# Optimization experiments

Hardware: AMD Instinct MI355X
Metric: run time of the kernel (lower is better)

## Reference

```python
import jax, jax.numpy as jnp
import numpy as np

K = 1024       # npoint (downsampled points)
NN = 16        # nneighbor (kNN group size)
EPS = 1e-5     # BatchNorm eps


def setup_inputs() -> dict:
    key = jax.random.key(0)
    ks = jax.random.split(key, 6)
    B, N, D = 8, 4096, 64          # channels[0] = D + 3 = 67
    C1, C2 = 128, 128              # mlp = channels[1:]
    xyz = jax.random.normal(ks[0], (B, N, 3), jnp.float32)
    points = jax.random.normal(ks[1], (B, N, D), jnp.float32)
    W1 = jax.random.normal(ks[2], (C1, D + 3), jnp.float32) / np.float32(np.sqrt(D + 3))
    b1 = jnp.zeros((C1,), jnp.float32)
    g1 = jnp.ones((C1,), jnp.float32)
    be1 = jnp.zeros((C1,), jnp.float32)
    W2 = jax.random.normal(ks[3], (C2, C1), jnp.float32) / np.float32(np.sqrt(C1))
    b2 = jnp.zeros((C2,), jnp.float32)
    g2 = jnp.ones((C2,), jnp.float32)
    be2 = jnp.zeros((C2,), jnp.float32)
    return {"xyz": xyz, "points": points, "W1": W1, "b1": b1, "g1": g1, "be1": be1,
            "W2": W2, "b2": b2, "g2": g2, "be2": be2}


def _fps(xyz, npoint):
    # Farthest point sampling: sequential selection via lax.scan.
    B, N, _ = xyz.shape
    def step(carry, _):
        dist, far = carry
        centroid = jnp.take_along_axis(xyz, far[:, None, None], axis=1)  # [B,1,3]
        d = jnp.sum((xyz - centroid) ** 2, axis=-1)                      # [B,N]
        dist = jnp.minimum(dist, d)
        return (dist, jnp.argmax(dist, axis=-1).astype(jnp.int32)), far
    init = (jnp.full((B, N), 1e10, xyz.dtype), jnp.zeros((B,), jnp.int32))
    _, idx = jax.lax.scan(step, init, None, length=npoint)
    return idx.T  # [B, npoint]


def _bn_relu(x, g, b):
    # training-mode BatchNorm2d over (batch, npoint, nsample), per channel (last dim)
    mean = jnp.mean(x, axis=(0, 1, 2), keepdims=True)
    var = jnp.var(x, axis=(0, 1, 2), keepdims=True)
    return jax.nn.relu((x - mean) * jax.lax.rsqrt(var + EPS) * g + b)


def reference(xyz, points, W1, b1, g1, be1, W2, b2, g2, be2):
    B, N, _ = xyz.shape
    fps_idx = _fps(xyz, K)                                  # [B,K]
    gather = jax.vmap(lambda a, i: a[i])
    new_xyz = gather(xyz, fps_idx)                          # [B,K,3]
    # kNN: squared distances from sampled centers to all points
    sq = (jnp.sum(new_xyz ** 2, -1)[:, :, None]
          + jnp.sum(xyz ** 2, -1)[:, None, :]
          - 2.0 * jnp.einsum('bkc,bnc->bkn', new_xyz, xyz))  # [B,K,N]
    _, knn_idx = jax.lax.top_k(-sq, NN)                     # [B,K,NN]
    grouped_xyz = gather(xyz, knn_idx)                      # [B,K,NN,3]
    grouped_xyz = grouped_xyz - new_xyz[:, :, None, :]
    grouped_pts = gather(points, knn_idx)                   # [B,K,NN,D]
    h = jnp.concatenate([grouped_xyz, grouped_pts], axis=-1)  # [B,K,NN,D+3]
    h = _bn_relu(jnp.einsum('bknc,oc->bkno', h, W1) + b1, g1, be1)
    h = _bn_relu(jnp.einsum('bknc,oc->bkno', h, W2) + b2, g2, be2)
    new_points = jnp.max(h, axis=2)                         # [B,K,C2]
    return new_xyz, new_points
```

## Files before the change

kernel.cpp:

```cpp
#include <hip/hip_runtime.h>

#define B_ 8
#define N_ 4096
#define K_ 1024
#define NN_ 16
#define C1_ 128
#define C2_ 128
#define CIN_ 67
#define NROWS (B_*K_*NN_)
#define NBLK  (NROWS/64)
#define NBLK2 (NROWS/32)
#define BN_N 131072.0f

typedef unsigned short u16;

__device__ u16   g_knn[NROWS];
__device__ float g_statsA[8*256];
__device__ float g_statsB[8*256];
__device__ float g_m2[B_*K_*C2_];
__device__ float g_W1T[68*128];
__device__ float g_W2T[128*128];
__device__ __align__(16) float g_h1[(size_t)NROWS*128];

template<int CTRL>
static __device__ __forceinline__ void dpp_maxv_step(float& v) {
    int vi = __float_as_int(v);
    int ov = __builtin_amdgcn_update_dpp(vi, vi, CTRL, 0xf, 0xf, false);
    v = fmaxf(v, __int_as_float(ov));
}
static __device__ __forceinline__ void wave_reduce_maxval(float& v) {
    dpp_maxv_step<0x111>(v);
    dpp_maxv_step<0x112>(v);
    dpp_maxv_step<0x114>(v);
    dpp_maxv_step<0x118>(v);
    dpp_maxv_step<0x142>(v);
    dpp_maxv_step<0x143>(v);
}
template<int CTRL>
static __device__ __forceinline__ void dpp_min_step(float& v, int& ib) {
    int vi = __float_as_int(v);
    int ov = __builtin_amdgcn_update_dpp(vi, vi, CTRL, 0xf, 0xf, false);
    int oi = __builtin_amdgcn_update_dpp(ib, ib, CTRL, 0xf, 0xf, false);
    float of = __int_as_float(ov);
    if (of < v || (of == v && oi < ib)) { v = of; ib = oi; }
}
static __device__ __forceinline__ void wave_reduce_min(float& v, int& ib) {
    dpp_min_step<0x111>(v, ib);
    dpp_min_step<0x112>(v, ib);
    dpp_min_step<0x114>(v, ib);
    dpp_min_step<0x118>(v, ib);
    dpp_min_step<0x142>(v, ib);
    dpp_min_step<0x143>(v, ib);
}

__global__ void transpose_w_kernel(const float* __restrict__ W1,
                                   const float* __restrict__ W2) {
    int t = blockIdx.x * 256 + threadIdx.x;
    if (t < 8*256) { g_statsA[t] = 0.f; g_statsB[t] = 0.f; }
    if (t < 68*128) {
        int q = t >> 7, o = t & 127;
        g_W1T[t] = (q < CIN_) ? W1[o*CIN_ + q] : 0.f;
    }
    if (t < 128*128) {
        int q = t >> 7, o = t & 127;
        g_W2T[t] = W2[o*C1_ + q];
    }
}

__global__ __launch_bounds__(256) void fps_kernel(const float* __restrict__ xyz,
                                                  float* __restrict__ out_xyz) {
    __shared__ float sx[N_*3];
    __shared__ float sout[K_*3];
    __shared__ float wv[2][4];
    __shared__ int   wi[2][4];
    const int b = blockIdx.x, t = threadIdx.x;
    const int l = t & 63, w = t >> 6;
    const float* xb = xyz + b * (N_ * 3);
    for (int e = t; e < N_*3; e += 256) sx[e] = xb[e];
    __syncthreads();
    float x0[16], y0[16], z0[16], dist[16];
    #pragma unroll
    for (int j = 0; j < 16; ++j) {
        int p = t * 16 + j;
        x0[j] = sx[p*3+0]; y0[j] = sx[p*3+1]; z0[j] = sx[p*3+2];
        dist[j] = 1e10f;
    }
    int far = 0;
    for (int s = 0; s < K_; ++s) {
        const float cx = sx[far*3+0], cy = sx[far*3+1], cz = sx[far*3+2];
        if (t == 0) {
            sout[s*3+0] = cx; sout[s*3+1] = cy; sout[s*3+2] = cz;
        }
        float v = -1.f; int ib = 0;
        {
            #pragma clang fp contract(fast)
            #pragma unroll
            for (int j = 0; j < 16; ++j) {
                float dx = x0[j]-cx, dy = y0[j]-cy, dz = z0[j]-cz;
                float dd = dx*dx + dy*dy + dz*dz;
                dd = fminf(dist[j], dd);
                dist[j] = dd;
                if (dd > v) { v = dd; ib = t*16 + j; }
            }
        }
        float vr = v;
        wave_reduce_maxval(vr);
        const float m = __int_as_float(__builtin_amdgcn_readlane(__float_as_int(vr), 63));
        unsigned long long mk = __ballot(v == m);
        const int ln  = __ffsll((unsigned long long)mk) - 1;
        const int wib = __builtin_amdgcn_readlane(ib, ln);
        const int pb = s & 1;
        if (l == 0) { wv[pb][w] = m; wi[pb][w] = wib; }
        __syncthreads();
        float bv = wv[pb][0]; int bi = wi[pb][0];
        #pragma unroll
        for (int ww = 1; ww < 4; ++ww) {
            float ov = wv[pb][ww];
            if (ov > bv) { bv = ov; bi = wi[pb][ww]; }
        }
        far = bi & 4095;
    }
    __syncthreads();
    for (int e = t; e < K_*3; e += 256) out_xyz[b*K_*3 + e] = sout[e];
}

__global__ __launch_bounds__(256) void knn_kernel(const float* __restrict__ xyz,
                                                  const float* __restrict__ newxyz) {
    __shared__ float px[N_], py[N_], pz[N_];
    const int b = blockIdx.y, t = threadIdx.x;
    const int l = t & 63, w = t >> 6;
    const int k = blockIdx.x * 4 + w;
    const int m = b*K_ + k;
    const float* xb = xyz + b * (N_ * 3);
    for (int p = t; p < N_; p += 256) {
        px[p] = xb[p*3+0]; py[p] = xb[p*3+1]; pz[p] = xb[p*3+2];
    }
    __syncthreads();
    const float cx = newxyz[m*3+0];
    const float cy = newxyz[m*3+1];
    const float cz = newxyz[m*3+2];
    float d[64];
    {
        #pragma clang fp contract(off)
        float sn = cx*cx; sn = sn + cy*cy; sn = sn + cz*cz;
        #pragma unroll
        for (int j = 0; j < 64; ++j) {
            int p = j*64 + l;
            float X = px[p], Y = py[p], Z = pz[p];
            float sp = X*X; sp = sp + Y*Y; sp = sp + Z*Z;
            float dt = cx*X; dt = dt + cy*Y; dt = dt + cz*Z;
            float t1 = sn + sp;
            d[j] = t1 - 2.0f*dt;
        }
    }
    float prevd = -1e38f; int previ = -1;
    for (int r = 0; r < NN_; ++r) {
        float bv = 1e38f; int bi = 0x7fffffff;
        #pragma unroll
        for (int j = 0; j < 64; ++j) {
            int p = j*64 + l;
            bool gt = (d[j] > prevd) || (d[j] == prevd && p > previ);
            bool lt = (d[j] < bv)   || (d[j] == bv   && p < bi);
            if (gt && lt) { bv = d[j]; bi = p; }
        }
        wave_reduce_min(bv, bi);
        previ = __builtin_amdgcn_readlane(bi, 63);
        prevd = __int_as_float(__builtin_amdgcn_readlane(__float_as_int(bv), 63));
        if (l == 0) g_knn[m*NN_ + r] = (u16)(previ & 4095);
    }
}

__global__ __launch_bounds__(256) void stats1_kernel(
        const float* __restrict__ xyz, const float* __restrict__ points,
        const float* __restrict__ newxyz, const float* __restrict__ b1) {
    __shared__ union {
        float Xs[64][68];
        struct { float ps[16][128], pq[16][128]; } c;
    } u;
    __shared__ float cen[4][3];
    __shared__ int rowp[64];
    const int t = threadIdx.x;
    const int blk = blockIdx.x;
    const int b = blk >> 8;
    const int g0 = blk * 64;
    if (t < 64)  rowp[t] = ((int)g_knn[g0 + t]) & 4095;
    if (t < 12)  cen[t/3][t%3] = newxyz[(blk*4 + t/3)*3 + (t%3)];
    __syncthreads();
    for (int e = t; e < 64*68; e += 256) {
        int r = e / 68, c = e % 68;
        int p = rowp[r];
        float v = 0.f;
        if (c < 3)         v = xyz[(b*N_ + p)*3 + c] - cen[r >> 4][c];
        else if (c < CIN_) v = points[(b*N_ + p)*64 + (c - 3)];
        u.Xs[r][c] = v;
    }
    __syncthreads();
    const int rg = t >> 4, cg = t & 15;
    const int r0 = rg * 4;
    float acc[4][8];
    #pragma unroll
    for (int j = 0; j < 4; ++j)
        #pragma unroll
        for (int i = 0; i < 8; ++i) acc[j][i] = 0.f;
    for (int q4 = 0; q4 < 17; ++q4) {
        float4 xv[4];
        #pragma unroll
        for (int j = 0; j < 4; ++j) xv[j] = *(const float4*)&u.Xs[r0 + j][q4*4];
        #pragma unroll
        for (int i = 0; i < 8; ++i) {
            int o = cg + 16*i;
            float w0 = g_W1T[(q4*4+0)*128 + o];
            float w1 = g_W1T[(q4*4+1)*128 + o];
            float w2 = g_W1T[(q4*4+2)*128 + o];
            float w3 = g_W1T[(q4*4+3)*128 + o];
            #pragma unroll
            for (int j = 0; j < 4; ++j) {
                float a = acc[j][i];
                a = a + xv[j].x*w0; a = a + xv[j].y*w1;
                a = a + xv[j].z*w2; a = a + xv[j].w*w3;
                acc[j][i] = a;
            }
        }
    }
    __syncthreads();
    #pragma unroll
    for (int i = 0; i < 8; ++i) {
        int o = cg + 16*i;
        float bias = b1[o];
        float s = 0.f, sq = 0.f;
        #pragma unroll
        for (int j = 0; j < 4; ++j) {
            float v = acc[j][i] + bias;
            g_h1[(size_t)(g0 + r0 + j)*128 + o] = v;
            s += v; sq += v*v;
        }
        u.c.ps[rg][o] = s; u.c.pq[rg][o] = sq;
    }
    __syncthreads();
    if (t < 128) {
        float ts = 0.f, tq = 0.f;
        #pragma unroll
        for (int g = 0; g < 16; ++g) { ts += u.c.ps[g][t]; tq += u.c.pq[g][t]; }
        const int slot = (blk & 7) * 256;
        atomicAdd(&g_statsA[slot + t], ts);
        atomicAdd(&g_statsA[slot + 128 + t], tq);
    }
}

__global__ __launch_bounds__(256) void gemm2_kernel(
        const float* __restrict__ b2, const float* __restrict__ g1,
        const float* __restrict__ be1) {
    __shared__ float mn1[128], sc1[128], bb1[128];
    __shared__ union {
        float h1s[32][132];
        struct { float ps[16][128], pq[16][128], pm[16][128]; } c;
    } u;
    const int t = threadIdx.x;
    const int blk = blockIdx.x;
    const int g0 = blk * 32;
    if (t < 128) {
        float sum = 0.f, sq = 0.f;
        #pragma unroll
        for (int s = 0; s < 8; ++s) {
            sum += g_statsA[s*256 + t];
            sq  += g_statsA[s*256 + 128 + t];
        }
        float mean = sum * (1.f / BN_N);
        float var  = sq * (1.f / BN_N) - mean*mean;
        mn1[t] = mean; sc1[t] = (1.f / sqrtf(var + 1e-5f)) * g1[t];
        bb1[t] = be1[t];
    }
    __syncthreads();
    for (int e = t*4; e < 32*128; e += 1024) {
        float4 hv = *(const float4*)&g_h1[(size_t)g0*128 + e];
        int r = e >> 7, c = e & 127;
        u.h1s[r][c+0] = fmaxf((hv.x - mn1[c+0])*sc1[c+0] + bb1[c+0], 0.f);
        u.h1s[r][c+1] = fmaxf((hv.y - mn1[c+1])*sc1[c+1] + bb1[c+1], 0.f);
        u.h1s[r][c+2] = fmaxf((hv.z - mn1[c+2])*sc1[c+2] + bb1[c+2], 0.f);
        u.h1s[r][c+3] = fmaxf((hv.w - mn1[c+3])*sc1[c+3] + bb1[c+3], 0.f);
    }
    __syncthreads();
    const int rg = t >> 4, cg = t & 15;
    const int r0 = rg * 2;
    float acc2[2][8];
    #pragma unroll
    for (int j = 0; j < 2; ++j)
        #pragma unroll
        for (int i = 0; i < 8; ++i) acc2[j][i] = 0.f;
    for (int q4 = 0; q4 < 32; ++q4) {
        float4 xv0 = *(const float4*)&u.h1s[r0][q4*4];
        float4 xv1 = *(const float4*)&u.h1s[r0+1][q4*4];
        #pragma unroll
        for (int i = 0; i < 8; ++i) {
            int o = cg + 16*i;
            float w0 = g_W2T[(q4*4+0)*128 + o];
            float w1 = g_W2T[(q4*4+1)*128 + o];
            float w2 = g_W2T[(q4*4+2)*128 + o];
            float w3 = g_W2T[(q4*4+3)*128 + o];
            float a0 = acc2[0][i];
            a0 = a0 + xv0.x*w0; a0 = a0 + xv0.y*w1;
            a0 = a0 + xv0.z*w2; a0 = a0 + xv0.w*w3;
            acc2[0][i] = a0;
            float a1 = acc2[1][i];
            a1 = a1 + xv1.x*w0; a1 = a1 + xv1.y*w1;
            a1 = a1 + xv1.z*w2; a1 = a1 + xv1.w*w3;
            acc2[1][i] = a1;
        }
    }
    __syncthreads();
    #pragma unroll
    for (int i = 0; i < 8; ++i) {
        int o = cg + 16*i;
        float bias = b2[o];
        float s = 0.f, sq = 0.f, mx = -1e38f;
        #pragma unroll
        for (int j = 0; j < 2; ++j) {
            float v = acc2[j][i] + bias;
            s += v; sq += v*v; mx = fmaxf(mx, v);
        }
        u.c.ps[rg][o] = s; u.c.pq[rg][o] = sq; u.c.pm[rg][o] = mx;
    }
    __syncthreads();
    if (t < 128) {
        float ts = 0.f, tq = 0.f;
        #pragma unroll
        for (int g = 0; g < 16; ++g) { ts += u.c.ps[g][t]; tq += u.c.pq[g][t]; }
        const int slot = (blk & 7) * 256;
        atomicAdd(&g_statsB[slot + t], ts);
        atomicAdd(&g_statsB[slot + 128 + t], tq);
    }
    {
        const int o = t & 127, gg = t >> 7;
        float mx = u.c.pm[gg*8 + 0][o];
        #pragma unroll
        for (int g = 1; g < 8; ++g) mx = fmaxf(mx, u.c.pm[gg*8 + g][o]);
        g_m2[(blk*2 + gg)*128 + o] = mx;
    }
}

__global__ __launch_bounds__(256) void final_kernel(
        const float* __restrict__ g2, const float* __restrict__ be2,
        float* __restrict__ outp) {
    __shared__ float mn[128], sc[128], bb[128];
    const int t = threadIdx.x;
    if (t < 128) {
        float sum = 0.f, sq = 0.f;
        #pragma unroll
        for (int s = 0; s < 8; ++s) {
            sum += g_statsB[s*256 + t];
            sq  += g_statsB[s*256 + 128 + t];
        }
        float mean = sum * (1.f / BN_N);
        float var  = sq * (1.f / BN_N) - mean*mean;
        float inv  = 1.f / sqrtf(var + 1e-5f);
        mn[t] = mean; sc[t] = inv * g2[t]; bb[t] = be2[t];
    }
    __syncthreads();
    const int m = blockIdx.x*2 + (t >> 7);
    const int c = t & 127;
    float v = (g_m2[m*128 + c] - mn[c]) * sc[c] + bb[c];
    v = fmaxf(v, 0.f);
    outp[m*C2_ + c] = v;
}

extern "C" void kernel_launch(void* const* d_in, const int* in_sizes, int n_in,
                              void* d_out, int out_size, void* d_ws, size_t ws_size,
                              hipStream_t stream) {
    const float* xyz    = (const float*)d_in[0];
    const float* points = (const float*)d_in[1];
    const float* W1     = (const float*)d_in[2];
    const float* b1     = (const float*)d_in[3];
    const float* g1     = (const float*)d_in[4];
    const float* be1    = (const float*)d_in[5];
    const float* W2     = (const float*)d_in[6];
    const float* b2     = (const float*)d_in[7];
    const float* g2     = (const float*)d_in[8];
    const float* be2    = (const float*)d_in[9];

    float* out_xyz = (float*)d_out;
    float* out_pts = (float*)d_out + B_*K_*3;

    (void)d_ws; (void)ws_size;

    transpose_w_kernel<<<64, 256, 0, stream>>>(W1, W2);
    fps_kernel<<<B_, 256, 0, stream>>>(xyz, out_xyz);
    knn_kernel<<<dim3(256, B_), 256, 0, stream>>>(xyz, out_xyz);
    stats1_kernel<<<NBLK, 256, 0, stream>>>(xyz, points, out_xyz, b1);
    gemm2_kernel<<<NBLK2, 256, 0, stream>>>(b2, g1, be1);
    final_kernel<<<B_*K_/2, 256, 0, stream>>>(g2, be2, out_pts);
}
```

Baseline: 1.104 ms.

## Process two batches per FPS block and carry centroid coordinates through reduction

The FPS kernel now handles two batches per block, interleaving their independent selection chains so the latency of each wave reduction and barrier is shared. The reduction carries the winning point's coordinates instead of its index, which removes the dependent shared-memory lookup of the next centroid and the shared staging of the input cloud. Outputs are written straight to global memory each step. The cost is doubled register pressure and half as many blocks (4 instead of 8), so less of the GPU is in use for this serial stage.

New measurement: 1.914 ms. 1.73x slower.

```diff
diff --git a/kernel.cpp b/kernel.cpp
--- a/kernel.cpp
+++ b/kernel.cpp
@@ -67,61 +67,85 @@
     }
 }
 
-__global__ __launch_bounds__(256) void fps_kernel(const float* __restrict__ xyz,
-                                                  float* __restrict__ out_xyz) {
-    __shared__ float sx[N_*3];
-    __shared__ float sout[K_*3];
-    __shared__ float wv[2][4];
-    __shared__ int   wi[2][4];
-    const int b = blockIdx.x, t = threadIdx.x;
+static __device__ __forceinline__ void fps_batch_step(
+        float cx, float cy, float cz,
+        float (&x0)[16], float (&y0)[16], float (&z0)[16], float (&dist)[16],
+        float4* wslot, int l) {
+    float v = -1.f, bx = 0.f, by = 0.f, bz = 0.f;
+    {
+        #pragma clang fp contract(fast)
+        #pragma unroll
+        for (int j = 0; j < 16; ++j) {
+            float dx = x0[j]-cx, dy = y0[j]-cy, dz = z0[j]-cz;
+            float dd = dx*dx + dy*dy + dz*dz;
+            dd = fminf(dist[j], dd);
+            dist[j] = dd;
+            if (dd > v) { v = dd; bx = x0[j]; by = y0[j]; bz = z0[j]; }
+        }
+    }
+    float vr = v;
+    wave_reduce_maxval(vr);
+    const float m = __int_as_float(__builtin_amdgcn_readlane(__float_as_int(vr), 63));
+    unsigned long long mk = __ballot(v == m);
+    const int ln = __ffsll(mk) - 1;
+    const float wbx = __int_as_float(__builtin_amdgcn_readlane(__float_as_int(bx), ln));
+    const float wby = __int_as_float(__builtin_amdgcn_readlane(__float_as_int(by), ln));
+    const float wbz = __int_as_float(__builtin_amdgcn_readlane(__float_as_int(bz), ln));
+    if (l == 0) *wslot = make_float4(m, wbx, wby, wbz);
+}
+
+__global__ __launch_bounds__(256, 1) void fps_kernel(const float* __restrict__ xyz,
+                                                     float* __restrict__ out_xyz) {
+    __shared__ float4 wred[2][2][4];
+    const int t = threadIdx.x;
     const int l = t & 63, w = t >> 6;
-    const float* xb = xyz + b * (N_ * 3);
-    for (int e = t; e < N_*3; e += 256) sx[e] = xb[e];
-    __syncthreads();
-    float x0[16], y0[16], z0[16], dist[16];
+    const int b0 = blockIdx.x * 2;
+    const float* xbA = xyz + (size_t)b0       * (N_ * 3);
+    const float* xbB = xyz + (size_t)(b0 + 1) * (N_ * 3);
+    float xA[16], yA[16], zA[16], dA[16];
+    float xB[16], yB[16], zB[16], dB[16];
     #pragma unroll
     for (int j = 0; j < 16; ++j) {
         int p = t * 16 + j;
-        x0[j] = sx[p*3+0]; y0[j] = sx[p*3+1]; z0[j] = sx[p*3+2];
-        dist[j] = 1e10f;
-    }
-    int far = 0;
+        xA[j] = xbA[p*3+0]; yA[j] = xbA[p*3+1]; zA[j] = xbA[p*3+2];
+        xB[j] = xbB[p*3+0]; yB[j] = xbB[p*3+1]; zB[j] = xbB[p*3+2];
+        dA[j] = 1e10f; dB[j] = 1e10f;
+    }
+    float cxA = xbA[0], cyA = xbA[1], czA = xbA[2];
+    float cxB = xbB[0], cyB = xbB[1], czB = xbB[2];
+
     for (int s = 0; s < K_; ++s) {
-        const float cx = sx[far*3+0], cy = sx[far*3+1], cz = sx[far*3+2];
         if (t == 0) {
-            sout[s*3+0] = cx; sout[s*3+1] = cy; sout[s*3+2] = cz;
-        }
-        float v = -1.f; int ib = 0;
+            float* o = out_xyz + ((size_t)b0*K_ + s)*3;
+            o[0] = cxA; o[1] = cyA; o[2] = czA;
+        }
+        if (t == 1) {
+            float* o = out_xyz + ((size_t)(b0+1)*K_ + s)*3;
+            o[0] = cxB; o[1] = cyB; o[2] = czB;
+        }
+        const int pb = s & 1;
+        fps_batch_step(cxA, cyA, czA, xA, yA, zA, dA, &wred[pb][0][w], l);
+        fps_batch_step(cxB, cyB, czB, xB, yB, zB, dB, &wred[pb][1][w], l);
+        __syncthreads();
         {
-            #pragma clang fp contract(fast)
+            float4 e = wred[pb][0][0];
+            float bv = e.x; cxA = e.y; cyA = e.z; czA = e.w;
             #pragma unroll
-            for (int j = 0; j < 16; ++j) {
-                float dx = x0[j]-cx, dy = y0[j]-cy, dz = z0[j]-cz;
-                float dd = dx*dx + dy*dy + dz*dz;
-                dd = fminf(dist[j], dd);
-                dist[j] = dd;
-                if (dd > v) { v = dd; ib = t*16 + j; }
+            for (int ww = 1; ww < 4; ++ww) {
+                float4 f = wred[pb][0][ww];
+                if (f.x > bv) { bv = f.x; cxA = f.y; cyA = f.z; czA = f.w; }
             }
         }
-        float vr = v;
-        wave_reduce_maxval(vr);
-        const float m = __int_as_float(__builtin_amdgcn_readlane(__float_as_int(vr), 63));
-        unsigned long long mk = __ballot(v == m);
-        const int ln  = __ffsll((unsigned long long)mk) - 1;
-        const int wib = __builtin_amdgcn_readlane(ib, ln);
-        const int pb = s & 1;
-        if (l == 0) { wv[pb][w] = m; wi[pb][w] = wib; }
-        __syncthreads();
-        float bv = wv[pb][0]; int bi = wi[pb][0];
-        #pragma unroll
-        for (int ww = 1; ww < 4; ++ww) {
-            float ov = wv[pb][ww];
-            if (ov > bv) { bv = ov; bi = wi[pb][ww]; }
-        }
-        far = bi & 4095;
-    }
-    __syncthreads();
-    for (int e = t; e < K_*3; e += 256) out_xyz[b*K_*3 + e] = sout[e];
+        {
+            float4 e = wred[pb][1][0];
+            float bv = e.x; cxB = e.y; cyB = e.z; czB = e.w;
+            #pragma unroll
+            for (int ww = 1; ww < 4; ++ww) {
+                float4 f = wred[pb][1][ww];
+                if (f.x > bv) { bv = f.x; cxB = f.y; cyB = f.z; czB = f.w; }
+            }
+        }
+    }
 }
 
 __global__ __launch_bounds__(256) void knn_kernel(const float* __restrict__ xyz,
@@ -383,7 +407,7 @@
     (void)d_ws; (void)ws_size;
 
     transpose_w_kernel<<<64, 256, 0, stream>>>(W1, W2);
-    fps_kernel<<<B_, 256, 0, stream>>>(xyz, out_xyz);
+    fps_kernel<<<B_/2, 256, 0, stream>>>(xyz, out_xyz);
     knn_kernel<<<dim3(256, B_), 256, 0, stream>>>(xyz, out_xyz);
     stats1_kernel<<<NBLK, 256, 0, stream>>>(xyz, points, out_xyz, b1);
     gemm2_kernel<<<NBLK2, 256, 0, stream>>>(b2, g1, be1);
```

## Widen FPS to 512 threads and carry winner coordinates through the reduction

Applied to the files above, without the earlier changes.

The farthest-point-sampling kernel now runs 512 threads with 8 points each instead of 256 with 16. Each lane carries the coordinates of its best candidate rather than its index, so the block-level reduction hands the next centroid straight to every thread and the dependent shared-memory lookup of the point cloud goes away. The full LDS copy of xyz and the staged output buffer are dropped, and centroids are written directly to global memory. The trade-off is a second wave-level barrier stage across 8 waves, plus extra readlanes per step.

Result: slower. 1.431 ms (+29.6%).

```diff
diff --git a/kernel.cpp b/kernel.cpp
--- a/kernel.cpp
+++ b/kernel.cpp
@@ -67,61 +67,58 @@
     }
 }
 
-__global__ __launch_bounds__(256) void fps_kernel(const float* __restrict__ xyz,
-                                                  float* __restrict__ out_xyz) {
-    __shared__ float sx[N_*3];
-    __shared__ float sout[K_*3];
-    __shared__ float wv[2][4];
-    __shared__ int   wi[2][4];
-    const int b = blockIdx.x, t = threadIdx.x;
+__global__ __launch_bounds__(512, 2) void fps_kernel(const float* __restrict__ xyz,
+                                                     float* __restrict__ out_xyz) {
+    __shared__ float4 wred[2][8];
+    const int t = threadIdx.x;
     const int l = t & 63, w = t >> 6;
-    const float* xb = xyz + b * (N_ * 3);
-    for (int e = t; e < N_*3; e += 256) sx[e] = xb[e];
-    __syncthreads();
-    float x0[16], y0[16], z0[16], dist[16];
-    #pragma unroll
-    for (int j = 0; j < 16; ++j) {
-        int p = t * 16 + j;
-        x0[j] = sx[p*3+0]; y0[j] = sx[p*3+1]; z0[j] = sx[p*3+2];
+    const int b = blockIdx.x;
+    const float* xb = xyz + (size_t)b * (N_ * 3);
+    float x0[8], y0[8], z0[8], dist[8];
+    #pragma unroll
+    for (int j = 0; j < 8; ++j) {
+        int p = t * 8 + j;
+        x0[j] = xb[p*3+0]; y0[j] = xb[p*3+1]; z0[j] = xb[p*3+2];
         dist[j] = 1e10f;
     }
-    int far = 0;
+    float cx = xb[0], cy = xb[1], cz = xb[2];
+
     for (int s = 0; s < K_; ++s) {
-        const float cx = sx[far*3+0], cy = sx[far*3+1], cz = sx[far*3+2];
         if (t == 0) {
-            sout[s*3+0] = cx; sout[s*3+1] = cy; sout[s*3+2] = cz;
-        }
-        float v = -1.f; int ib = 0;
+            float* o = out_xyz + ((size_t)b*K_ + s)*3;
+            o[0] = cx; o[1] = cy; o[2] = cz;
+        }
+        float v = -1.f, bx = 0.f, by = 0.f, bz = 0.f;
         {
             #pragma clang fp contract(fast)
             #pragma unroll
-            for (int j = 0; j < 16; ++j) {
+            for (int j = 0; j < 8; ++j) {
                 float dx = x0[j]-cx, dy = y0[j]-cy, dz = z0[j]-cz;
                 float dd = dx*dx + dy*dy + dz*dz;
                 dd = fminf(dist[j], dd);
                 dist[j] = dd;
-                if (dd > v) { v = dd; ib = t*16 + j; }
+                if (dd > v) { v = dd; bx = x0[j]; by = y0[j]; bz = z0[j]; }
             }
         }
         float vr = v;
         wave_reduce_maxval(vr);
         const float m = __int_as_float(__builtin_amdgcn_readlane(__float_as_int(vr), 63));
         unsigned long long mk = __ballot(v == m);
-        const int ln  = __ffsll((unsigned long long)mk) - 1;
-        const int wib = __builtin_amdgcn_readlane(ib, ln);
+        const int ln = __ffsll(mk) - 1;
+        const float wbx = __int_as_float(__builtin_amdgcn_readlane(__float_as_int(bx), ln));
+        const float wby = __int_as_float(__builtin_amdgcn_readlane(__float_as_int(by), ln));
+        const float wbz = __int_as_float(__builtin_amdgcn_readlane(__float_as_int(bz), ln));
         const int pb = s & 1;
-        if (l == 0) { wv[pb][w] = m; wi[pb][w] = wib; }
+        if (l == 0) wred[pb][w] = make_float4(m, wbx, wby, wbz);
         __syncthreads();
-        float bv = wv[pb][0]; int bi = wi[pb][0];
-        #pragma unroll
-        for (int ww = 1; ww < 4; ++ww) {
-            float ov = wv[pb][ww];
-            if (ov > bv) { bv = ov; bi = wi[pb][ww]; }
-        }
-        far = bi & 4095;
-    }
-    __syncthreads();
-    for (int e = t; e < K_*3; e += 256) out_xyz[b*K_*3 + e] = sout[e];
+        float4 e = wred[pb][0];
+        float bv = e.x; cx = e.y; cy = e.z; cz = e.w;
+        #pragma unroll
+        for (int ww = 1; ww < 8; ++ww) {
+            float4 f = wred[pb][ww];
+            if (f.x > bv) { bv = f.x; cx = f.y; cy = f.z; cz = f.w; }
+        }
+    }
 }
 
 __global__ __launch_bounds__(256) void knn_kernel(const float* __restrict__ xyz,
@@ -383,7 +380,7 @@
     (void)d_ws; (void)ws_size;
 
     transpose_w_kernel<<<64, 256, 0, stream>>>(W1, W2);
-    fps_kernel<<<B_, 256, 0, stream>>>(xyz, out_xyz);
+    fps_kernel<<<B_, 512, 0, stream>>>(xyz, out_xyz);
     knn_kernel<<<dim3(256, B_), 256, 0, stream>>>(xyz, out_xyz);
     stats1_kernel<<<NBLK, 256, 0, stream>>>(xyz, points, out_xyz, b1);
     gemm2_kernel<<<NBLK2, 256, 0, stream>>>(b2, g1, be1);
```
